# Performance work log

Measured on AMD Instinct MI355X. Metric: run time of the kernel, lower is better.

## Reference

```python
import jax, jax.numpy as jnp
import numpy as np

MASK_VAL = -2.0**32 + 1.0

def setup_inputs() -> dict:
    key = jax.random.key(0)
    ks = jax.random.split(key, 8)
    B, T, E = 4096, 200, 64
    H1, H2 = 64, 32
    return {
        "query": jax.random.normal(ks[0], (B, 1, E), dtype=jnp.float32),
        "keys": jax.random.normal(ks[1], (B, T, E), dtype=jnp.float32),
        "keys_len": jax.random.randint(ks[2], (B, 1), 0, T, dtype=jnp.int64),
        "W1": jax.random.normal(ks[3], (4 * E, H1), dtype=jnp.float32) * 0.05,
        "b1": jnp.zeros((H1,), dtype=jnp.float32),
        "W2": jax.random.normal(ks[4], (H1, H2), dtype=jnp.float32) * 0.05,
        "b2": jnp.zeros((H2,), dtype=jnp.float32),
        "W3": jax.random.normal(ks[5], (H2, 1), dtype=jnp.float32) * 0.05,
        "b3": jnp.zeros((1,), dtype=jnp.float32),
    }

def reference(query, keys, keys_len, W1, b1, W2, b2, W3, b3):
    B, T, E = keys.shape
    q = jnp.broadcast_to(query, (B, T, E))                      # (B,T,E)
    x = jnp.concatenate([q, keys, q - keys, q * keys], axis=-1)  # (B,T,4E)
    h = jax.nn.relu(jnp.einsum('bti,ih->bth', x, W1) + b1)       # (B,T,H1)
    h = jax.nn.relu(jnp.einsum('bth,ho->bto', h, W2) + b2)       # (B,T,H2)
    score = jnp.einsum('bto,oc->btc', h, W3) + b3                # (B,T,1)
    score = jnp.transpose(score, (0, 2, 1))                      # (B,1,T)
    mask = (jnp.arange(T)[None, :] < keys_len)[:, None, :]       # (B,1,T)
    scores = jnp.where(mask, score, jnp.float32(MASK_VAL))
    scores = jax.nn.softmax(scores, axis=-1)                     # weight_normalization=True
    return jnp.matmul(scores, keys)                              # (B,1,E)
```

## Files before the change

### kernel.cpp

```cpp
#include <hip/hip_runtime.h>

typedef __attribute__((ext_vector_type(8))) short short8_t;
typedef __attribute__((ext_vector_type(4))) float f32x4;

#define MASK_VAL (-4294967295.0f)
#define NEG_BIG  (-1e30f)

__device__ __forceinline__ short f2bf(float x) {
    unsigned u;
    __builtin_memcpy(&u, &x, 4);
    u += 0x7FFFu + ((u >> 16) & 1u);
    return (short)(u >> 16);
}
__device__ __forceinline__ float bf2f(short s) {
    unsigned u = ((unsigned)(unsigned short)s) << 16;
    float f;
    __builtin_memcpy(&f, &u, 4);
    return f;
}

__global__ __launch_bounds__(256) void prep_all(
    const float* __restrict__ W1, const float* __restrict__ W2,
    const float* __restrict__ query, const float* __restrict__ b1,
    void* __restrict__ ws, int B)
{
    short* wkT = (short*)ws;
    short* wdT = wkT + 4096;
    short* w2T = wkT + 8192;
    float* csAll = (float*)((char*)ws + 36864);
    const int tid = threadIdx.x;

    if (blockIdx.x == 0) {
        for (int idx = tid; idx < 4096; idx += 256) {
            int n = idx & 63, k = idx >> 6;
            float a  = W1[4096  + idx];
            float c  = W1[8192  + idx];
            float d  = W1[12288 + idx];
            wkT[n * 64 + k] = f2bf(a - c);
            wdT[n * 64 + k] = f2bf(d);
        }
        for (int idx = tid; idx < 2048; idx += 256) {
            int o = idx & 31, h = idx >> 5;
            w2T[o * 64 + h] = f2bf(W2[idx]);
        }
        return;
    }

    __shared__ float wacs[4096];
    __shared__ float qsb[16 * 64];
    __shared__ float b1s[64];
    const int g0 = (blockIdx.x - 1) * 16;
    for (int idx = tid; idx < 4096; idx += 256)
        wacs[idx] = W1[idx] + W1[8192 + idx];
    {
        int nb = B - g0; if (nb > 16) nb = 16;
        if (nb > 0)
            for (int i = tid; i < nb * 16; i += 256)
                ((float4*)qsb)[i] = ((const float4*)(query + (size_t)g0 * 64))[i];
    }
    if (tid < 64) b1s[tid] = b1[tid];
    __syncthreads();
    for (int o = tid; o < 1024; o += 256) {
        int bb = o >> 6, h = o & 63;
        if (g0 + bb >= B) continue;
        float acc = b1s[h];
#pragma unroll 16
        for (int i = 0; i < 64; ++i)
            acc += qsb[bb * 64 + i] * wacs[i * 64 + h];
        csAll[(size_t)(g0 + bb) * 64 + h] = acc;
    }
}

__global__ __launch_bounds__(256, 2) void attn_main(
    const float* __restrict__ query,
    const float* __restrict__ keys,
    const int*   __restrict__ keys_len,
    const float* __restrict__ b2,
    const float* __restrict__ W3,
    const float* __restrict__ b3,
    const void*  __restrict__ ws,
    float* __restrict__ out,
    int B)
{
    constexpr int STR = 72;
    const short* wkT   = (const short*)ws;
    const short* wdT   = wkT + 4096;
    const short* w2T   = wkT + 8192;
    const float* csAll = (const float*)((const char*)ws + 36864);

    __shared__ short Bk[64 * STR];
    __shared__ short Bd[64 * STR];
    __shared__ short W2s[32 * STR];
    __shared__ short h1w[4][16 * STR];

    const int tid  = threadIdx.x;
    const int lane = tid & 63;
    const int wid  = tid >> 6;
    const int col  = lane & 15;
    const int quad = lane >> 4;
    const int b    = blockIdx.x * 4 + wid;
    const bool act = (b < B);

    for (int c = tid; c < 512; c += 256) {
        int r = c >> 3, ch = (c & 7) * 8;
        *(short8_t*)&Bk[r * STR + ch] = *(const short8_t*)(wkT + r * 64 + ch);
        *(short8_t*)&Bd[r * STR + ch] = *(const short8_t*)(wdT + r * 64 + ch);
    }
    {
        int r = tid >> 3, ch = (tid & 7) * 8;
        *(short8_t*)&W2s[r * STR + ch] = *(const short8_t*)(w2T + r * 64 + ch);
    }

    const float* kb = nullptr;
    float4 pA0, pA1, pA2, pA3;
    float4 pB0, pB1, pB2, pB3;
    float4 qv0, qv1, qv2, qv3;
    float4 b2qa, b2qb, w3qa, w3qb;
    float cs0 = 0.f, cs1 = 0.f, cs2 = 0.f, cs3 = 0.f, b3v = 0.f;
    if (act) {
        kb = keys + (size_t)b * 12800;
        {
            const float* kr = kb + col * 64 + quad * 8;
            pA0 = *(const float4*)(kr);
            pA1 = *(const float4*)(kr + 4);
            pA2 = *(const float4*)(kr + 32);
            pA3 = *(const float4*)(kr + 36);
        }
        {
            const float* kr = kb + (16 + col) * 64 + quad * 8;
            pB0 = *(const float4*)(kr);
            pB1 = *(const float4*)(kr + 4);
            pB2 = *(const float4*)(kr + 32);
            pB3 = *(const float4*)(kr + 36);
        }
        const float* qb = query + (size_t)b * 64;
        qv0 = *(const float4*)(qb + quad * 8);
        qv1 = *(const float4*)(qb + quad * 8 + 4);
        qv2 = *(const float4*)(qb + 32 + quad * 8);
        qv3 = *(const float4*)(qb + 32 + quad * 8 + 4);
        const float* cb = csAll + (size_t)b * 64;
        cs0 = cb[col]; cs1 = cb[16 + col]; cs2 = cb[32 + col]; cs3 = cb[48 + col];
        b2qa = *(const float4*)(b2 + quad * 4);
        b2qb = *(const float4*)(b2 + 16 + quad * 4);
        w3qa = *(const float4*)(W3 + quad * 4);
        w3qb = *(const float4*)(W3 + 16 + quad * 4);
        b3v  = b3[0];
    }
    __syncthreads();
    if (!act) return;

    const int len = keys_len[b];
    short* hw = h1w[wid];

    float m_ln = NEG_BIG, l_ln = 0.f;
    float accv[16];
#pragma unroll
    for (int i = 0; i < 16; ++i) accv[i] = 0.f;

    auto tile = [&](int jt, float4 k0, float4 k1, float4 k2, float4 k3) {
        short8_t aK0, aK1, aQ0, aQ1;
        aK0[0] = f2bf(k0.x); aK0[1] = f2bf(k0.y); aK0[2] = f2bf(k0.z); aK0[3] = f2bf(k0.w);
        aK0[4] = f2bf(k1.x); aK0[5] = f2bf(k1.y); aK0[6] = f2bf(k1.z); aK0[7] = f2bf(k1.w);
        aK1[0] = f2bf(k2.x); aK1[1] = f2bf(k2.y); aK1[2] = f2bf(k2.z); aK1[3] = f2bf(k2.w);
        aK1[4] = f2bf(k3.x); aK1[5] = f2bf(k3.y); aK1[6] = f2bf(k3.z); aK1[7] = f2bf(k3.w);
        aQ0[0] = f2bf(k0.x * qv0.x); aQ0[1] = f2bf(k0.y * qv0.y);
        aQ0[2] = f2bf(k0.z * qv0.z); aQ0[3] = f2bf(k0.w * qv0.w);
        aQ0[4] = f2bf(k1.x * qv1.x); aQ0[5] = f2bf(k1.y * qv1.y);
        aQ0[6] = f2bf(k1.z * qv1.z); aQ0[7] = f2bf(k1.w * qv1.w);
        aQ1[0] = f2bf(k2.x * qv2.x); aQ1[1] = f2bf(k2.y * qv2.y);
        aQ1[2] = f2bf(k2.z * qv2.z); aQ1[3] = f2bf(k2.w * qv2.w);
        aQ1[4] = f2bf(k3.x * qv3.x); aQ1[5] = f2bf(k3.y * qv3.y);
        aQ1[6] = f2bf(k3.z * qv3.z); aQ1[7] = f2bf(k3.w * qv3.w);

        f32x4 acc[4] = {f32x4{0,0,0,0}, f32x4{0,0,0,0}, f32x4{0,0,0,0}, f32x4{0,0,0,0}};
#pragma unroll
        for (int nt = 0; nt < 4; ++nt) {
            const short* bp = &Bk[(nt * 16 + col) * STR + quad * 8];
            const short* dp = &Bd[(nt * 16 + col) * STR + quad * 8];
            acc[nt] = __builtin_amdgcn_mfma_f32_16x16x32_bf16(aK0, *(const short8_t*)bp,        acc[nt], 0, 0, 0);
            acc[nt] = __builtin_amdgcn_mfma_f32_16x16x32_bf16(aK1, *(const short8_t*)(bp + 32), acc[nt], 0, 0, 0);
            acc[nt] = __builtin_amdgcn_mfma_f32_16x16x32_bf16(aQ0, *(const short8_t*)dp,        acc[nt], 0, 0, 0);
            acc[nt] = __builtin_amdgcn_mfma_f32_16x16x32_bf16(aQ1, *(const short8_t*)(dp + 32), acc[nt], 0, 0, 0);
        }

        float csv[4] = {cs0, cs1, cs2, cs3};
#pragma unroll
        for (int nt = 0; nt < 4; ++nt) {
            float cadd = csv[nt];
#pragma unroll
            for (int r = 0; r < 4; ++r)
                hw[(quad * 4 + r) * STR + nt * 16 + col] = f2bf(fmaxf(acc[nt][r] + cadd, 0.f));
        }

        f32x4 acc2a = f32x4{b2qa.x, b2qa.y, b2qa.z, b2qa.w};
        f32x4 acc2b = f32x4{b2qb.x, b2qb.y, b2qb.z, b2qb.w};
#pragma unroll
        for (int ks = 0; ks < 2; ++ks) {
            short8_t h1f = *(const short8_t*)&hw[col * STR + ks * 32 + quad * 8];
            acc2a = __builtin_amdgcn_mfma_f32_16x16x32_bf16(
                *(const short8_t*)&W2s[col * STR + ks * 32 + quad * 8],        h1f, acc2a, 0, 0, 0);
            acc2b = __builtin_amdgcn_mfma_f32_16x16x32_bf16(
                *(const short8_t*)&W2s[(16 + col) * STR + ks * 32 + quad * 8], h1f, acc2b, 0, 0, 0);
        }

        float sp = 0.f;
#pragma unroll
        for (int r = 0; r < 4; ++r) {
            sp += fmaxf(acc2a[r], 0.f) * w3qa[r]
                + fmaxf(acc2b[r], 0.f) * w3qb[r];
        }
        sp += __shfl_xor(sp, 16);
        sp += __shfl_xor(sp, 32);
        float sv = sp + b3v;

        int   row  = jt * 16 + col;
        bool  vrow = row < 200;
        float sval = (row < len) ? sv : MASK_VAL;
        float m_new = vrow ? fmaxf(m_ln, sval) : m_ln;
        float scale = __expf(m_ln - m_new);
        float p     = vrow ? __expf(sval - m_new) : 0.f;
        m_ln = m_new;
        l_ln = l_ln * scale + p;
#pragma unroll
        for (int i = 0; i < 8; ++i) {
            accv[i]     = accv[i]     * scale + p * bf2f(aK0[i]);
            accv[8 + i] = accv[8 + i] * scale + p * bf2f(aK1[i]);
        }
    };

#pragma unroll 1
    for (int i = 0; i < 6; ++i) {
        const int jt = i * 2;
        float4 c0 = pA0, c1 = pA1, c2 = pA2, c3 = pA3;
        {
            int row = (jt + 2) * 16 + col;
            row = row < 200 ? row : 199;
            const float* kr = kb + row * 64 + quad * 8;
            pA0 = *(const float4*)(kr);
            pA1 = *(const float4*)(kr + 4);
            pA2 = *(const float4*)(kr + 32);
            pA3 = *(const float4*)(kr + 36);
        }
        tile(jt, c0, c1, c2, c3);
        float4 d0 = pB0, d1 = pB1, d2 = pB2, d3 = pB3;
        {
            int row = (jt + 3) * 16 + col;
            row = row < 200 ? row : 199;
            const float* kr = kb + row * 64 + quad * 8;
            pB0 = *(const float4*)(kr);
            pB1 = *(const float4*)(kr + 4);
            pB2 = *(const float4*)(kr + 32);
            pB3 = *(const float4*)(kr + 36);
        }
        tile(jt + 1, d0, d1, d2, d3);
    }
    tile(12, pA0, pA1, pA2, pA3);

    float mg = m_ln;
    mg = fmaxf(mg, __shfl_xor(mg, 1));
    mg = fmaxf(mg, __shfl_xor(mg, 2));
    mg = fmaxf(mg, __shfl_xor(mg, 4));
    mg = fmaxf(mg, __shfl_xor(mg, 8));
    float corr = __expf(m_ln - mg);
    float lg = l_ln * corr;
    lg += __shfl_xor(lg, 1);
    lg += __shfl_xor(lg, 2);
    lg += __shfl_xor(lg, 4);
    lg += __shfl_xor(lg, 8);
    float inv = 1.f / lg;
#pragma unroll
    for (int i = 0; i < 16; ++i) {
        float v = accv[i] * corr;
        v += __shfl_xor(v, 1);
        v += __shfl_xor(v, 2);
        v += __shfl_xor(v, 4);
        v += __shfl_xor(v, 8);
        accv[i] = v * inv;
    }
    if (col == 0) {
        float* op = out + (size_t)b * 64;
        *(float4*)(op + quad * 8)          = make_float4(accv[0],  accv[1],  accv[2],  accv[3]);
        *(float4*)(op + quad * 8 + 4)      = make_float4(accv[4],  accv[5],  accv[6],  accv[7]);
        *(float4*)(op + 32 + quad * 8)     = make_float4(accv[8],  accv[9],  accv[10], accv[11]);
        *(float4*)(op + 32 + quad * 8 + 4) = make_float4(accv[12], accv[13], accv[14], accv[15]);
    }
}

extern "C" void kernel_launch(void* const* d_in, const int* in_sizes, int n_in,
                              void* d_out, int out_size, void* d_ws, size_t ws_size,
                              hipStream_t stream) {
    const float* query    = (const float*)d_in[0];
    const float* keys     = (const float*)d_in[1];
    const int*   keys_len = (const int*)d_in[2];
    const float* W1       = (const float*)d_in[3];
    const float* b1       = (const float*)d_in[4];
    const float* W2       = (const float*)d_in[5];
    const float* b2       = (const float*)d_in[6];
    const float* W3       = (const float*)d_in[7];
    const float* b3       = (const float*)d_in[8];
    float* out            = (float*)d_out;

    const int B = in_sizes[1] / 12800;

    prep_all<<<dim3(1 + (B + 15) / 16), dim3(256), 0, stream>>>(W1, W2, query, b1, d_ws, B);
    attn_main<<<dim3((B + 3) / 4), dim3(256), 0, stream>>>(
        query, keys, keys_len, b2, W3, b3, d_ws, out, B);
}
```

Before: 319.8 us.

## Fold query into per-batch effective key weights, halving layer-1 MFMAs

Because the q*k term is linear in k for a fixed query, each wave now builds its own effective weight matrix Wk + q⊙Wd in LDS at kernel start. The per-tile q*k products and two of the four MFMAs per output tile are removed. This costs a per-wave 64x64 weight build, extra bf16 rounding of the combined weights, and four times the LDS for weights. Launch bounds are also raised to 3 blocks per CU.

Result: slower. 349.7 us (+9.4%).

```diff
diff --git a/kernel.cpp b/kernel.cpp
--- a/kernel.cpp
+++ b/kernel.cpp
@@ -71,7 +71,7 @@
     }
 }
 
-__global__ __launch_bounds__(256, 2) void attn_main(
+__global__ __launch_bounds__(256, 3) void attn_main(
     const float* __restrict__ query,
     const float* __restrict__ keys,
     const int*   __restrict__ keys_len,
@@ -88,8 +88,7 @@
     const short* w2T   = wkT + 8192;
     const float* csAll = (const float*)((const char*)ws + 36864);
 
-    __shared__ short Bk[64 * STR];
-    __shared__ short Bd[64 * STR];
+    __shared__ short Wq[4][64 * STR];
     __shared__ short W2s[32 * STR];
     __shared__ short h1w[4][16 * STR];
 
@@ -101,11 +100,6 @@
     const int b    = blockIdx.x * 4 + wid;
     const bool act = (b < B);
 
-    for (int c = tid; c < 512; c += 256) {
-        int r = c >> 3, ch = (c & 7) * 8;
-        *(short8_t*)&Bk[r * STR + ch] = *(const short8_t*)(wkT + r * 64 + ch);
-        *(short8_t*)&Bd[r * STR + ch] = *(const short8_t*)(wdT + r * 64 + ch);
-    }
     {
         int r = tid >> 3, ch = (tid & 7) * 8;
         *(short8_t*)&W2s[r * STR + ch] = *(const short8_t*)(w2T + r * 64 + ch);
@@ -114,7 +108,6 @@
     const float* kb = nullptr;
     float4 pA0, pA1, pA2, pA3;
     float4 pB0, pB1, pB2, pB3;
-    float4 qv0, qv1, qv2, qv3;
     float4 b2qa, b2qb, w3qa, w3qb;
     float cs0 = 0.f, cs1 = 0.f, cs2 = 0.f, cs3 = 0.f, b3v = 0.f;
     if (act) {
@@ -133,11 +126,29 @@
             pB2 = *(const float4*)(kr + 32);
             pB3 = *(const float4*)(kr + 36);
         }
-        const float* qb = query + (size_t)b * 64;
-        qv0 = *(const float4*)(qb + quad * 8);
-        qv1 = *(const float4*)(qb + quad * 8 + 4);
-        qv2 = *(const float4*)(qb + 32 + quad * 8);
-        qv3 = *(const float4*)(qb + 32 + quad * 8 + 4);
+        {
+            const float* qb = query + (size_t)b * 64;
+            short* wqr = &Wq[wid][lane * STR];
+            const short* wkr = wkT + lane * 64;
+            const short* wdr = wdT + lane * 64;
+#pragma unroll
+            for (int g = 0; g < 8; ++g) {
+                float4 qa = *(const float4*)(qb + g * 8);
+                float4 qc = *(const float4*)(qb + g * 8 + 4);
+                short8_t wk8 = *(const short8_t*)(wkr + g * 8);
+                short8_t wd8 = *(const short8_t*)(wdr + g * 8);
+                short8_t o;
+                o[0] = f2bf(bf2f(wk8[0]) + qa.x * bf2f(wd8[0]));
+                o[1] = f2bf(bf2f(wk8[1]) + qa.y * bf2f(wd8[1]));
+                o[2] = f2bf(bf2f(wk8[2]) + qa.z * bf2f(wd8[2]));
+                o[3] = f2bf(bf2f(wk8[3]) + qa.w * bf2f(wd8[3]));
+                o[4] = f2bf(bf2f(wk8[4]) + qc.x * bf2f(wd8[4]));
+                o[5] = f2bf(bf2f(wk8[5]) + qc.y * bf2f(wd8[5]));
+                o[6] = f2bf(bf2f(wk8[6]) + qc.z * bf2f(wd8[6]));
+                o[7] = f2bf(bf2f(wk8[7]) + qc.w * bf2f(wd8[7]));
+                *(short8_t*)(wqr + g * 8) = o;
+            }
+        }
         const float* cb = csAll + (size_t)b * 64;
         cs0 = cb[col]; cs1 = cb[16 + col]; cs2 = cb[32 + col]; cs3 = cb[48 + col];
         b2qa = *(const float4*)(b2 + quad * 4);
@@ -151,6 +162,7 @@
 
     const int len = keys_len[b];
     short* hw = h1w[wid];
+    const short* wq = Wq[wid];
 
     float m_ln = NEG_BIG, l_ln = 0.f;
     float accv[16];
@@ -158,29 +170,18 @@
     for (int i = 0; i < 16; ++i) accv[i] = 0.f;
 
     auto tile = [&](int jt, float4 k0, float4 k1, float4 k2, float4 k3) {
-        short8_t aK0, aK1, aQ0, aQ1;
+        short8_t aK0, aK1;
         aK0[0] = f2bf(k0.x); aK0[1] = f2bf(k0.y); aK0[2] = f2bf(k0.z); aK0[3] = f2bf(k0.w);
         aK0[4] = f2bf(k1.x); aK0[5] = f2bf(k1.y); aK0[6] = f2bf(k1.z); aK0[7] = f2bf(k1.w);
         aK1[0] = f2bf(k2.x); aK1[1] = f2bf(k2.y); aK1[2] = f2bf(k2.z); aK1[3] = f2bf(k2.w);
         aK1[4] = f2bf(k3.x); aK1[5] = f2bf(k3.y); aK1[6] = f2bf(k3.z); aK1[7] = f2bf(k3.w);
-        aQ0[0] = f2bf(k0.x * qv0.x); aQ0[1] = f2bf(k0.y * qv0.y);
-        aQ0[2] = f2bf(k0.z * qv0.z); aQ0[3] = f2bf(k0.w * qv0.w);
-        aQ0[4] = f2bf(k1.x * qv1.x); aQ0[5] = f2bf(k1.y * qv1.y);
-        aQ0[6] = f2bf(k1.z * qv1.z); aQ0[7] = f2bf(k1.w * qv1.w);
-        aQ1[0] = f2bf(k2.x * qv2.x); aQ1[1] = f2bf(k2.y * qv2.y);
-        aQ1[2] = f2bf(k2.z * qv2.z); aQ1[3] = f2bf(k2.w * qv2.w);
-        aQ1[4] = f2bf(k3.x * qv3.x); aQ1[5] = f2bf(k3.y * qv3.y);
-        aQ1[6] = f2bf(k3.z * qv3.z); aQ1[7] = f2bf(k3.w * qv3.w);
 
         f32x4 acc[4] = {f32x4{0,0,0,0}, f32x4{0,0,0,0}, f32x4{0,0,0,0}, f32x4{0,0,0,0}};
 #pragma unroll
         for (int nt = 0; nt < 4; ++nt) {
-            const short* bp = &Bk[(nt * 16 + col) * STR + quad * 8];
-            const short* dp = &Bd[(nt * 16 + col) * STR + quad * 8];
+            const short* bp = &wq[(nt * 16 + col) * STR + quad * 8];
             acc[nt] = __builtin_amdgcn_mfma_f32_16x16x32_bf16(aK0, *(const short8_t*)bp,        acc[nt], 0, 0, 0);
             acc[nt] = __builtin_amdgcn_mfma_f32_16x16x32_bf16(aK1, *(const short8_t*)(bp + 32), acc[nt], 0, 0, 0);
-            acc[nt] = __builtin_amdgcn_mfma_f32_16x16x32_bf16(aQ0, *(const short8_t*)dp,        acc[nt], 0, 0, 0);
-            acc[nt] = __builtin_amdgcn_mfma_f32_16x16x32_bf16(aQ1, *(const short8_t*)(dp + 32), acc[nt], 0, 0, 0);
         }
 
         float csv[4] = {cs0, cs1, cs2, cs3};
```
